# Optimization experiments

Measured on AMD Instinct MI355X. Metric: run time of the kernel, lower is better.

The kernel has to match this reference:

```python
import jax, jax.numpy as jnp
from jax import lax
import numpy as np

B, L, D = 16, 512, 256
F, K = 256, 3
M = 2048
EPS = 1e-5


def setup_inputs() -> dict:
    key = jax.random.key(0)
    ks = jax.random.split(key, 12)
    x = jax.random.normal(ks[0], (B, L, D), jnp.float32)
    # integer durations >= 1, sum over L <= 3*512 = 1536 < M, as in training targets
    target = jax.random.randint(ks[1], (B, L), 1, 4)
    s = 0.02
    conv1_w = jax.random.normal(ks[2], (F, D, K), jnp.float32) * s
    conv1_b = jnp.zeros((F,), jnp.float32)
    ln1_g = jnp.ones((F,), jnp.float32)
    ln1_b = jnp.zeros((F,), jnp.float32)
    conv2_w = jax.random.normal(ks[3], (F, F, K), jnp.float32) * s
    conv2_b = jnp.zeros((F,), jnp.float32)
    ln2_g = jnp.ones((F,), jnp.float32)
    ln2_b = jnp.zeros((F,), jnp.float32)
    lin_w = jax.random.normal(ks[4], (F, 1), jnp.float32) * s
    lin_b = jnp.zeros((1,), jnp.float32)
    return dict(x=x, target=target, mel_max_length=M,
                conv1_w=conv1_w, conv1_b=conv1_b, ln1_g=ln1_g, ln1_b=ln1_b,
                conv2_w=conv2_w, conv2_b=conv2_b, ln2_g=ln2_g, ln2_b=ln2_b,
                lin_w=lin_w, lin_b=lin_b)


def _layer_norm(h, g, b):
    mu = jnp.mean(h, axis=-1, keepdims=True)
    var = jnp.mean(jnp.square(h - mu), axis=-1, keepdims=True)
    return (h - mu) * lax.rsqrt(var + EPS) * g + b


def _conv1d(h_bld, w, b):
    # h: (B, L, C_in), w: (C_out, C_in, K) -> (B, L, C_out), SAME padding
    pad = (w.shape[-1] - 1) // 2
    h = jnp.transpose(h_bld, (0, 2, 1))  # (B, C, L)
    h = lax.conv_general_dilated(h, w, (1,), [(pad, pad)],
                                 dimension_numbers=('NCH', 'OIH', 'NCH'))
    return jnp.transpose(h + b[None, :, None], (0, 2, 1))


def _duration_predictor(x, conv1_w, conv1_b, ln1_g, ln1_b,
                        conv2_w, conv2_b, ln2_g, ln2_b, lin_w, lin_b):
    # FastSpeech duration predictor (eval mode: dropout = identity)
    h = jax.nn.relu(_layer_norm(_conv1d(x, conv1_w, conv1_b), ln1_g, ln1_b))
    h = jax.nn.relu(_layer_norm(_conv1d(h, conv2_w, conv2_b), ln2_g, ln2_b))
    return jax.nn.relu(h @ lin_w + lin_b)[..., 0]  # (B, L)


def _length_regulate(x, dur, mel_max_length):
    # alignment[b,m,l] = 1 iff cs[l-1] <= m < cs[l]  (exactly the scatter+diff trick
    # of create_alignment, padded to mel_max_length as in the original F.pad)
    cs = jnp.cumsum(dur, axis=1)              # (B, L) inclusive cumsum
    prev = cs - dur                           # exclusive cumsum
    m = jnp.arange(mel_max_length)[None, :, None]  # (1, M, 1)
    align = ((m >= prev[:, None, :]) & (m < cs[:, None, :])).astype(x.dtype)  # (B,M,L)
    return jnp.einsum('bml,bld->bmd', align, x)


def reference(x, target, mel_max_length, conv1_w, conv1_b, ln1_g, ln1_b,
              conv2_w, conv2_b, ln2_g, ln2_b, lin_w, lin_b):
    dup = _duration_predictor(x, conv1_w, conv1_b, ln1_g, ln1_b,
                              conv2_w, conv2_b, ln2_g, ln2_b, lin_w, lin_b)
    output = _length_regulate(x, target, mel_max_length)
    return (output, dup)
```

## Files before the change

kernel.cpp:

```cpp
#include <hip/hip_runtime.h>
#include <hip/hip_bf16.h>

#define Bn 16
#define Ln 512
#define Cn 256
#define Fn 256
#define Kn 3
#define Mn 2048

#define NKSTEP 24
#define MT 32
#define XS_PS 264
#define XROWS 50
#define HROWS 48
#define HOFF  8
#define NCONVBLK 256

typedef __attribute__((ext_vector_type(8))) short short8;
typedef __attribute__((ext_vector_type(4))) float f32x4;

static __device__ __forceinline__ unsigned short f2bf(float f) {
    unsigned int u = __float_as_uint(f);
    return (unsigned short)((u + 0x7fff + ((u >> 16) & 1)) >> 16);
}

__global__ __launch_bounds__(256) void pack_scan(
    const float* __restrict__ w1, const float* __restrict__ w2,
    unsigned short* __restrict__ bp1, unsigned short* __restrict__ bp2,
    const int* __restrict__ target, int* __restrict__ map)
{
    __shared__ int ss[256];
    const int blk = blockIdx.x;
    const int t = threadIdx.x;
    if (blk < 16) {
        const int bb = blk;
        int v0 = target[bb * Ln + 2 * t];
        int v1 = target[bb * Ln + 2 * t + 1];
        ss[t] = v0 + v1;
        __syncthreads();
        for (int off = 1; off < 256; off <<= 1) {
            int add = (t >= off) ? ss[t - off] : 0;
            __syncthreads();
            ss[t] += add;
            __syncthreads();
        }
        int S     = ss[t];
        int total = ss[255];
        int cs1   = S;
        int cs0   = S - v1;
        int prev0 = cs0 - v0;
        for (int m = prev0; m < cs0; ++m) map[bb * Mn + m] = 2 * t;
        for (int m = cs0;   m < cs1; ++m) map[bb * Mn + m] = 2 * t + 1;
        for (int m = total + t; m < Mn; m += 256) map[bb * Mn + m] = -1;
    } else {
        int v = (blk - 16) * 256 + t;
        const float* w = w1;
        unsigned short* bp = bp1;
        if (v >= 24576) { v -= 24576; w = w2; bp = bp2; }
        int lane = v & 63, nt = (v >> 6) & 15, s = v >> 10;
        int f    = nt * 16 + (lane & 15);
        int kap0 = s * 32 + (lane >> 4) * 8;
        const float* p = w + ((size_t)f * Cn + (kap0 & 255)) * Kn + (kap0 >> 8);
        short8 o;
        #pragma unroll
        for (int j = 0; j < 8; ++j) o[j] = (short)f2bf(p[3 * j]);
        *(short8*)(bp + (size_t)v * 8) = o;
    }
}

__global__ __launch_bounds__(256, 4) void conv12_gather(
    const float* __restrict__ x,
    const unsigned short* __restrict__ bp1,
    const unsigned short* __restrict__ bp2,
    const float* __restrict__ c1b, const float* __restrict__ g1, const float* __restrict__ be1,
    const float* __restrict__ c2b, const float* __restrict__ g2, const float* __restrict__ be2,
    const float* __restrict__ lw,  const float* __restrict__ lb,
    const int* __restrict__ gmap,
    float* __restrict__ out,
    float* __restrict__ dup)
{
    __shared__ __align__(16) unsigned short xs[XROWS * XS_PS];
    __shared__ float2 red[HROWS][4];
    __shared__ float  red2[MT][4];

    const int t = threadIdx.x;

    if (blockIdx.x >= NCONVBLK) {
        int e4 = (blockIdx.x - NCONVBLK) * 256 + t;
        int d4 = e4 & 63;
        int bm = e4 >> 6;
        int b  = bm >> 11;
        int l  = gmap[bm];
        float4 val = make_float4(0.f, 0.f, 0.f, 0.f);
        if (l >= 0) val = *((const float4*)(x + (size_t)(b * Ln + l) * Cn) + d4);
        ((float4*)out)[e4] = val;
        return;
    }

    const int b  = blockIdx.x >> 4;
    const int l0 = (blockIdx.x & 15) * MT;

    for (int idx = t; idx < XROWS * 64; idx += 256) {
        int row = idx >> 6;
        int c4  = (idx & 63) * 4;
        int l = l0 - 9 + row;
        float4 v = make_float4(0.f, 0.f, 0.f, 0.f);
        if (l >= 0 && l < Ln) v = *(const float4*)&x[((size_t)b * Ln + l) * Cn + c4];
        unsigned int lo = (unsigned int)f2bf(v.x) | ((unsigned int)f2bf(v.y) << 16);
        unsigned int hi = (unsigned int)f2bf(v.z) | ((unsigned int)f2bf(v.w) << 16);
        *(uint2*)&xs[row * XS_PS + c4] = make_uint2(lo, hi);
    }
    __syncthreads();

    const int lane = t & 63;
    const int wv   = t >> 6;
    const int mrow = lane & 15;
    const int q    = lane >> 4;

    f32x4  acc1[3][4] = {};
    short8 bfr[2][4];
    short8 afr[2][3];

    auto loadB1 = [&](int s, int slot) {
        const unsigned short* p = bp1 + (size_t)((s * 16 + wv * 4) * 64 + lane) * 8;
        #pragma unroll
        for (int i = 0; i < 4; ++i)
            bfr[slot][i] = *(const short8*)(p + (size_t)i * 64 * 8);
    };
    auto loadA1 = [&](int s, int slot) {
        const int k    = s >> 3;
        const int dcol = (s & 7) * 32 + q * 8;
        #pragma unroll
        for (int mt = 0; mt < 3; ++mt)
            afr[slot][mt] = *(const short8*)&xs[(mt * 16 + mrow + k) * XS_PS + dcol];
    };

    loadB1(0, 0); loadA1(0, 0);
    loadB1(1, 1); loadA1(1, 1);

    #pragma unroll 2
    for (int s = 0; s < NKSTEP; ++s) {
        const int slot = s & 1;
        #pragma unroll
        for (int mt = 0; mt < 3; ++mt)
            #pragma unroll
            for (int i = 0; i < 4; ++i)
                acc1[mt][i] = __builtin_amdgcn_mfma_f32_16x16x32_bf16(
                    afr[slot][mt], bfr[slot][i], acc1[mt][i], 0, 0, 0);
        const int sn = (s + 2 < NKSTEP) ? (s + 2) : s;
        loadB1(sn, slot);
        loadA1(sn, slot);
    }

    {
        float gv[4], bv[4], biasv[4];
        #pragma unroll
        for (int i = 0; i < 4; ++i) {
            int col = wv * 64 + i * 16 + mrow;
            biasv[i] = c1b[col];
            gv[i]    = g1[col];
            bv[i]    = be1[col];
        }
        #pragma unroll
        for (int mt = 0; mt < 3; ++mt)
            #pragma unroll
            for (int i = 0; i < 4; ++i)
                #pragma unroll
                for (int r = 0; r < 4; ++r)
                    acc1[mt][i][r] += biasv[i];

        #pragma unroll
        for (int mt = 0; mt < 3; ++mt)
            #pragma unroll
            for (int r = 0; r < 4; ++r) {
                float s  = acc1[mt][0][r] + acc1[mt][1][r] + acc1[mt][2][r] + acc1[mt][3][r];
                float sq = acc1[mt][0][r] * acc1[mt][0][r] + acc1[mt][1][r] * acc1[mt][1][r]
                         + acc1[mt][2][r] * acc1[mt][2][r] + acc1[mt][3][r] * acc1[mt][3][r];
                #pragma unroll
                for (int off = 1; off <= 8; off <<= 1) {
                    s  += __shfl_xor(s,  off, 64);
                    sq += __shfl_xor(sq, off, 64);
                }
                if (mrow == 0) red[mt * 16 + q * 4 + r][wv] = make_float2(s, sq);
            }
        __syncthreads();

        float muv[3][4], rsv[3][4];
        #pragma unroll
        for (int mt = 0; mt < 3; ++mt)
            #pragma unroll
            for (int r = 0; r < 4; ++r) {
                int row = mt * 16 + q * 4 + r;
                float2 p0 = red[row][0], p1 = red[row][1], p2 = red[row][2], p3 = red[row][3];
                float s  = p0.x + p1.x + p2.x + p3.x;
                float sq = p0.y + p1.y + p2.y + p3.y;
                float mu  = s * (1.f / 256.f);
                float var = sq * (1.f / 256.f) - mu * mu;
                muv[mt][r] = mu;
                rsv[mt][r] = rsqrtf(var + 1e-5f);
            }

        #pragma unroll
        for (int mt = 0; mt < 3; ++mt)
            #pragma unroll
            for (int r = 0; r < 4; ++r) {
                int jr = mt * 16 + q * 4 + r;
                int l  = l0 - HOFF + jr;
                bool ok = (l >= 0 && l < Ln);
                #pragma unroll
                for (int i = 0; i < 4; ++i) {
                    float o = ok ? fmaxf((acc1[mt][i][r] - muv[mt][r]) * rsv[mt][r] * gv[i] + bv[i], 0.f)
                                 : 0.f;
                    xs[jr * XS_PS + (wv * 64 + i * 16 + mrow)] = f2bf(o);
                }
            }
    }
    __syncthreads();

    f32x4  acc2[2][4] = {};
    short8 afr2[2][2];

    auto loadB2 = [&](int s, int slot) {
        const unsigned short* p = bp2 + (size_t)((s * 16 + wv * 4) * 64 + lane) * 8;
        #pragma unroll
        for (int i = 0; i < 4; ++i)
            bfr[slot][i] = *(const short8*)(p + (size_t)i * 64 * 8);
    };
    auto loadA2 = [&](int s, int slot) {
        const int k    = s >> 3;
        const int dcol = (s & 7) * 32 + q * 8;
        #pragma unroll
        for (int mt = 0; mt < 2; ++mt)
            afr2[slot][mt] = *(const short8*)&xs[(mt * 16 + mrow + k + 7) * XS_PS + dcol];
    };

    loadB2(0, 0); loadA2(0, 0);
    loadB2(1, 1); loadA2(1, 1);

    #pragma unroll 2
    for (int s = 0; s < NKSTEP; ++s) {
        const int slot = s & 1;
        #pragma unroll
        for (int mt = 0; mt < 2; ++mt)
            #pragma unroll
            for (int i = 0; i < 4; ++i)
                acc2[mt][i] = __builtin_amdgcn_mfma_f32_16x16x32_bf16(
                    afr2[slot][mt], bfr[slot][i], acc2[mt][i], 0, 0, 0);
        const int sn = (s + 2 < NKSTEP) ? (s + 2) : s;
        loadB2(sn, slot);
        loadA2(sn, slot);
    }

    {
        float gv[4], bv[4], biasv[4], lwv[4];
        #pragma unroll
        for (int i = 0; i < 4; ++i) {
            int col = wv * 64 + i * 16 + mrow;
            biasv[i] = c2b[col];
            gv[i]    = g2[col];
            bv[i]    = be2[col];
            lwv[i]   = lw[col];
        }
        #pragma unroll
        for (int mt = 0; mt < 2; ++mt)
            #pragma unroll
            for (int i = 0; i < 4; ++i)
                #pragma unroll
                for (int r = 0; r < 4; ++r)
                    acc2[mt][i][r] += biasv[i];

        #pragma unroll
        for (int mt = 0; mt < 2; ++mt)
            #pragma unroll
            for (int r = 0; r < 4; ++r) {
                float s  = acc2[mt][0][r] + acc2[mt][1][r] + acc2[mt][2][r] + acc2[mt][3][r];
                float sq = acc2[mt][0][r] * acc2[mt][0][r] + acc2[mt][1][r] * acc2[mt][1][r]
                         + acc2[mt][2][r] * acc2[mt][2][r] + acc2[mt][3][r] * acc2[mt][3][r];
                #pragma unroll
                for (int off = 1; off <= 8; off <<= 1) {
                    s  += __shfl_xor(s,  off, 64);
                    sq += __shfl_xor(sq, off, 64);
                }
                if (mrow == 0) red[mt * 16 + q * 4 + r][wv] = make_float2(s, sq);
            }
        __syncthreads();

        float muv[2][4], rsv[2][4];
        #pragma unroll
        for (int mt = 0; mt < 2; ++mt)
            #pragma unroll
            for (int r = 0; r < 4; ++r) {
                int row = mt * 16 + q * 4 + r;
                float2 p0 = red[row][0], p1 = red[row][1], p2 = red[row][2], p3 = red[row][3];
                float s  = p0.x + p1.x + p2.x + p3.x;
                float sq = p0.y + p1.y + p2.y + p3.y;
                float mu  = s * (1.f / 256.f);
                float var = sq * (1.f / 256.f) - mu * mu;
                muv[mt][r] = mu;
                rsv[mt][r] = rsqrtf(var + 1e-5f);
            }

        #pragma unroll
        for (int mt = 0; mt < 2; ++mt)
            #pragma unroll
            for (int r = 0; r < 4; ++r) {
                float dot = 0.f;
                #pragma unroll
                for (int i = 0; i < 4; ++i) {
                    float o = fmaxf((acc2[mt][i][r] - muv[mt][r]) * rsv[mt][r] * gv[i] + bv[i], 0.f);
                    dot += o * lwv[i];
                }
                #pragma unroll
                for (int off = 1; off <= 8; off <<= 1)
                    dot += __shfl_xor(dot, off, 64);
                if (mrow == 0) red2[mt * 16 + q * 4 + r][wv] = dot;
            }
        __syncthreads();
        if (t < MT) {
            float d = red2[t][0] + red2[t][1] + red2[t][2] + red2[t][3];
            dup[b * Ln + l0 + t] = fmaxf(d + lb[0], 0.f);
        }
    }
}

extern "C" void kernel_launch(void* const* d_in, const int* in_sizes, int n_in,
                              void* d_out, int out_size, void* d_ws, size_t ws_size,
                              hipStream_t stream) {
    const float* x    = (const float*)d_in[0];
    const int*   targ = (const int*)d_in[1];
    const float* c1w = (const float*)d_in[3];
    const float* c1b = (const float*)d_in[4];
    const float* g1  = (const float*)d_in[5];
    const float* be1 = (const float*)d_in[6];
    const float* c2w = (const float*)d_in[7];
    const float* c2b = (const float*)d_in[8];
    const float* g2  = (const float*)d_in[9];
    const float* be2 = (const float*)d_in[10];
    const float* lw  = (const float*)d_in[11];
    const float* lb  = (const float*)d_in[12];

    float* out     = (float*)d_out;
    float* out_dup = out + (size_t)Bn * Mn * Cn;

    char* ws = (char*)d_ws;
    unsigned short* bp1 = (unsigned short*)ws;
    unsigned short* bp2 = (unsigned short*)(ws + 393216);
    int*            map = (int*)(ws + 2 * 393216);

    pack_scan<<<208, 256, 0, stream>>>(c1w, c2w, bp1, bp2, targ, map);

    conv12_gather<<<NCONVBLK + (Bn * Mn * Cn / 4) / 256, 256, 0, stream>>>(
        x, bp1, bp2, c1b, g1, be1, c2b, g2, be2, lw, lb,
        map, out, out_dup);
}
```

Baseline: 132.7 us.

## Use 512-thread blocks: 8 waves split conv N-dim, gather does 4 float4 per thread

Doubles the block size to 512 threads so each conv block uses eight waves, each covering 32 output channels instead of 64. This halves per-wave accumulator and B-fragment registers, and the LayerNorm reductions now combine eight partials. The gather part shrinks from 8192 blocks to 1024, with each thread issuing four independent float4 gathers strided across the output. The aims are more wave-level parallelism in the conv and less block-launch overhead in the gather, at the cost of more redundant A-fragment LDS reads and wider cross-wave reductions.

Result: faster. 121.4 us (-8.5%).

```diff
diff --git a/kernel.cpp b/kernel.cpp
--- a/kernel.cpp
+++ b/kernel.cpp
@@ -15,6 +15,7 @@
 #define HROWS 48
 #define HOFF  8
 #define NCONVBLK 256
+#define NGATHERBLK 1024
 
 typedef __attribute__((ext_vector_type(8))) short short8;
 typedef __attribute__((ext_vector_type(4))) float f32x4;
@@ -68,7 +69,7 @@
     }
 }
 
-__global__ __launch_bounds__(256, 4) void conv12_gather(
+__global__ __launch_bounds__(512) void conv12_gather(
     const float* __restrict__ x,
     const unsigned short* __restrict__ bp1,
     const unsigned short* __restrict__ bp2,
@@ -80,27 +81,37 @@
     float* __restrict__ dup)
 {
     __shared__ __align__(16) unsigned short xs[XROWS * XS_PS];
-    __shared__ float2 red[HROWS][4];
-    __shared__ float  red2[MT][4];
+    __shared__ float2 red[HROWS][8];
+    __shared__ float  red2[MT][8];
 
     const int t = threadIdx.x;
 
     if (blockIdx.x >= NCONVBLK) {
-        int e4 = (blockIdx.x - NCONVBLK) * 256 + t;
-        int d4 = e4 & 63;
-        int bm = e4 >> 6;
-        int b  = bm >> 11;
-        int l  = gmap[bm];
-        float4 val = make_float4(0.f, 0.f, 0.f, 0.f);
-        if (l >= 0) val = *((const float4*)(x + (size_t)(b * Ln + l) * Cn) + d4);
-        ((float4*)out)[e4] = val;
+        const int base = (blockIdx.x - NCONVBLK) * 512 + t;
+        int lv[4];
+        #pragma unroll
+        for (int i = 0; i < 4; ++i)
+            lv[i] = gmap[(base + i * 524288) >> 6];
+        float4 val[4];
+        #pragma unroll
+        for (int i = 0; i < 4; ++i) {
+            int e4 = base + i * 524288;
+            int d4 = e4 & 63;
+            int b  = e4 >> 17;
+            val[i] = make_float4(0.f, 0.f, 0.f, 0.f);
+            if (lv[i] >= 0)
+                val[i] = *((const float4*)(x + (size_t)(b * Ln + lv[i]) * Cn) + d4);
+        }
+        #pragma unroll
+        for (int i = 0; i < 4; ++i)
+            ((float4*)out)[base + i * 524288] = val[i];
         return;
     }
 
     const int b  = blockIdx.x >> 4;
     const int l0 = (blockIdx.x & 15) * MT;
 
-    for (int idx = t; idx < XROWS * 64; idx += 256) {
+    for (int idx = t; idx < XROWS * 64; idx += 512) {
         int row = idx >> 6;
         int c4  = (idx & 63) * 4;
         int l = l0 - 9 + row;
@@ -117,46 +128,47 @@
     const int mrow = lane & 15;
     const int q    = lane >> 4;
 
-    f32x4  acc1[3][4] = {};
-    short8 bfr[2][4];
-    short8 afr[2][3];
-
-    auto loadB1 = [&](int s, int slot) {
-        const unsigned short* p = bp1 + (size_t)((s * 16 + wv * 4) * 64 + lane) * 8;
-        #pragma unroll
-        for (int i = 0; i < 4; ++i)
-            bfr[slot][i] = *(const short8*)(p + (size_t)i * 64 * 8);
-    };
-    auto loadA1 = [&](int s, int slot) {
-        const int k    = s >> 3;
-        const int dcol = (s & 7) * 32 + q * 8;
-        #pragma unroll
-        for (int mt = 0; mt < 3; ++mt)
-            afr[slot][mt] = *(const short8*)&xs[(mt * 16 + mrow + k) * XS_PS + dcol];
-    };
-
-    loadB1(0, 0); loadA1(0, 0);
-    loadB1(1, 1); loadA1(1, 1);
-
-    #pragma unroll 2
-    for (int s = 0; s < NKSTEP; ++s) {
-        const int slot = s & 1;
-        #pragma unroll
-        for (int mt = 0; mt < 3; ++mt)
-            #pragma unroll
-            for (int i = 0; i < 4; ++i)
-                acc1[mt][i] = __builtin_amdgcn_mfma_f32_16x16x32_bf16(
-                    afr[slot][mt], bfr[slot][i], acc1[mt][i], 0, 0, 0);
-        const int sn = (s + 2 < NKSTEP) ? (s + 2) : s;
-        loadB1(sn, slot);
-        loadA1(sn, slot);
-    }
-
+    f32x4  acc1[3][2] = {};
     {
-        float gv[4], bv[4], biasv[4];
-        #pragma unroll
-        for (int i = 0; i < 4; ++i) {
-            int col = wv * 64 + i * 16 + mrow;
+        short8 bfr[2][2];
+        short8 afr[2][3];
+
+        auto loadB1 = [&](int s, int slot) {
+            const unsigned short* p = bp1 + (size_t)((s * 16 + wv * 2) * 64 + lane) * 8;
+            bfr[slot][0] = *(const short8*)p;
+            bfr[slot][1] = *(const short8*)(p + 64 * 8);
+        };
+        auto loadA1 = [&](int s, int slot) {
+            const int k    = s >> 3;
+            const int dcol = (s & 7) * 32 + q * 8;
+            #pragma unroll
+            for (int mt = 0; mt < 3; ++mt)
+                afr[slot][mt] = *(const short8*)&xs[(mt * 16 + mrow + k) * XS_PS + dcol];
+        };
+
+        loadB1(0, 0); loadA1(0, 0);
+        loadB1(1, 1); loadA1(1, 1);
+
+        #pragma unroll 2
+        for (int s = 0; s < NKSTEP; ++s) {
+            const int slot = s & 1;
+            #pragma unroll
+            for (int mt = 0; mt < 3; ++mt)
+                #pragma unroll
+                for (int i = 0; i < 2; ++i)
+                    acc1[mt][i] = __builtin_amdgcn_mfma_f32_16x16x32_bf16(
+                        afr[slot][mt], bfr[slot][i], acc1[mt][i], 0, 0, 0);
+            const int sn = (s + 2 < NKSTEP) ? (s + 2) : s;
+            loadB1(sn, slot);
+            loadA1(sn, slot);
+        }
+    }
+
+    {
+        float gv[2], bv[2], biasv[2];
+        #pragma unroll
+        for (int i = 0; i < 2; ++i) {
+            int col = wv * 32 + i * 16 + mrow;
             biasv[i] = c1b[col];
             gv[i]    = g1[col];
             bv[i]    = be1[col];
@@ -164,7 +176,7 @@
         #pragma unroll
         for (int mt = 0; mt < 3; ++mt)
             #pragma unroll
-            for (int i = 0; i < 4; ++i)
+            for (int i = 0; i < 2; ++i)
                 #pragma unroll
                 for (int r = 0; r < 4; ++r)
                     acc1[mt][i][r] += biasv[i];
@@ -173,9 +185,8 @@
         for (int mt = 0; mt < 3; ++mt)
             #pragma unroll
             for (int r = 0; r < 4; ++r) {
-                float s  = acc1[mt][0][r] + acc1[mt][1][r] + acc1[mt][2][r] + acc1[mt][3][r];
-                float sq = acc1[mt][0][r] * acc1[mt][0][r] + acc1[mt][1][r] * acc1[mt][1][r]
-                         + acc1[mt][2][r] * acc1[mt][2][r] + acc1[mt][3][r] * acc1[mt][3][r];
+                float s  = acc1[mt][0][r] + acc1[mt][1][r];
+                float sq = acc1[mt][0][r] * acc1[mt][0][r] + acc1[mt][1][r] * acc1[mt][1][r];
                 #pragma unroll
                 for (int off = 1; off <= 8; off <<= 1) {
                     s  += __shfl_xor(s,  off, 64);
@@ -191,9 +202,12 @@
             #pragma unroll
             for (int r = 0; r < 4; ++r) {
                 int row = mt * 16 + q * 4 + r;
-                float2 p0 = red[row][0], p1 = red[row][1], p2 = red[row][2], p3 = red[row][3];
-                float s  = p0.x + p1.x + p2.x + p3.x;
-                float sq = p0.y + p1.y + p2.y + p3.y;
+                float s = 0.f, sq = 0.f;
+                #pragma unroll
+                for (int w = 0; w < 8; ++w) {
+                    float2 pp = red[row][w];
+                    s += pp.x; sq += pp.y;
+                }
                 float mu  = s * (1.f / 256.f);
                 float var = sq * (1.f / 256.f) - mu * mu;
                 muv[mt][r] = mu;
@@ -208,54 +222,56 @@
                 int l  = l0 - HOFF + jr;
                 bool ok = (l >= 0 && l < Ln);
                 #pragma unroll
-                for (int i = 0; i < 4; ++i) {
+                for (int i = 0; i < 2; ++i) {
                     float o = ok ? fmaxf((acc1[mt][i][r] - muv[mt][r]) * rsv[mt][r] * gv[i] + bv[i], 0.f)
                                  : 0.f;
-                    xs[jr * XS_PS + (wv * 64 + i * 16 + mrow)] = f2bf(o);
+                    xs[jr * XS_PS + (wv * 32 + i * 16 + mrow)] = f2bf(o);
                 }
             }
     }
     __syncthreads();
 
-    f32x4  acc2[2][4] = {};
-    short8 afr2[2][2];
-
-    auto loadB2 = [&](int s, int slot) {
-        const unsigned short* p = bp2 + (size_t)((s * 16 + wv * 4) * 64 + lane) * 8;
-        #pragma unroll
-        for (int i = 0; i < 4; ++i)
-            bfr[slot][i] = *(const short8*)(p + (size_t)i * 64 * 8);
-    };
-    auto loadA2 = [&](int s, int slot) {
-        const int k    = s >> 3;
-        const int dcol = (s & 7) * 32 + q * 8;
-        #pragma unroll
-        for (int mt = 0; mt < 2; ++mt)
-            afr2[slot][mt] = *(const short8*)&xs[(mt * 16 + mrow + k + 7) * XS_PS + dcol];
-    };
-
-    loadB2(0, 0); loadA2(0, 0);
-    loadB2(1, 1); loadA2(1, 1);
-
-    #pragma unroll 2
-    for (int s = 0; s < NKSTEP; ++s) {
-        const int slot = s & 1;
-        #pragma unroll
-        for (int mt = 0; mt < 2; ++mt)
-            #pragma unroll
-            for (int i = 0; i < 4; ++i)
-                acc2[mt][i] = __builtin_amdgcn_mfma_f32_16x16x32_bf16(
-                    afr2[slot][mt], bfr[slot][i], acc2[mt][i], 0, 0, 0);
-        const int sn = (s + 2 < NKSTEP) ? (s + 2) : s;
-        loadB2(sn, slot);
-        loadA2(sn, slot);
-    }
-
+    f32x4  acc2[2][2] = {};
     {
-        float gv[4], bv[4], biasv[4], lwv[4];
-        #pragma unroll
-        for (int i = 0; i < 4; ++i) {
-            int col = wv * 64 + i * 16 + mrow;
+        short8 bfr[2][2];
+        short8 afr[2][2];
+
+        auto loadB2 = [&](int s, int slot) {
+            const unsigned short* p = bp2 + (size_t)((s * 16 + wv * 2) * 64 + lane) * 8;
+            bfr[slot][0] = *(const short8*)p;
+            bfr[slot][1] = *(const short8*)(p + 64 * 8);
+        };
+        auto loadA2 = [&](int s, int slot) {
+            const int k    = s >> 3;
+            const int dcol = (s & 7) * 32 + q * 8;
+            #pragma unroll
+            for (int mt = 0; mt < 2; ++mt)
+                afr[slot][mt] = *(const short8*)&xs[(mt * 16 + mrow + k + 7) * XS_PS + dcol];
+        };
+
+        loadB2(0, 0); loadA2(0, 0);
+        loadB2(1, 1); loadA2(1, 1);
+
+        #pragma unroll 2
+        for (int s = 0; s < NKSTEP; ++s) {
+            const int slot = s & 1;
+            #pragma unroll
+            for (int mt = 0; mt < 2; ++mt)
+                #pragma unroll
+                for (int i = 0; i < 2; ++i)
+                    acc2[mt][i] = __builtin_amdgcn_mfma_f32_16x16x32_bf16(
+                        afr[slot][mt], bfr[slot][i], acc2[mt][i], 0, 0, 0);
+            const int sn = (s + 2 < NKSTEP) ? (s + 2) : s;
+            loadB2(sn, slot);
+            loadA2(sn, slot);
+        }
+    }
+
+    {
+        float gv[2], bv[2], biasv[2], lwv[2];
+        #pragma unroll
+        for (int i = 0; i < 2; ++i) {
+            int col = wv * 32 + i * 16 + mrow;
             biasv[i] = c2b[col];
             gv[i]    = g2[col];
             bv[i]    = be2[col];
@@ -264,7 +280,7 @@
         #pragma unroll
         for (int mt = 0; mt < 2; ++mt)
             #pragma unroll
-            for (int i = 0; i < 4; ++i)
+            for (int i = 0; i < 2; ++i)
                 #pragma unroll
                 for (int r = 0; r < 4; ++r)
                     acc2[mt][i][r] += biasv[i];
@@ -273,9 +289,8 @@
         for (int mt = 0; mt < 2; ++mt)
             #pragma unroll
             for (int r = 0; r < 4; ++r) {
-                float s  = acc2[mt][0][r] + acc2[mt][1][r] + acc2[mt][2][r] + acc2[mt][3][r];
-                float sq = acc2[mt][0][r] * acc2[mt][0][r] + acc2[mt][1][r] * acc2[mt][1][r]
-                         + acc2[mt][2][r] * acc2[mt][2][r] + acc2[mt][3][r] * acc2[mt][3][r];
+                float s  = acc2[mt][0][r] + acc2[mt][1][r];
+                float sq = acc2[mt][0][r] * acc2[mt][0][r] + acc2[mt][1][r] * acc2[mt][1][r];
                 #pragma unroll
                 for (int off = 1; off <= 8; off <<= 1) {
                     s  += __shfl_xor(s,  off, 64);
@@ -291,9 +306,12 @@
             #pragma unroll
             for (int r = 0; r < 4; ++r) {
                 int row = mt * 16 + q * 4 + r;
-                float2 p0 = red[row][0], p1 = red[row][1], p2 = red[row][2], p3 = red[row][3];
-                float s  = p0.x + p1.x + p2.x + p3.x;
-                float sq = p0.y + p1.y + p2.y + p3.y;
+                float s = 0.f, sq = 0.f;
+                #pragma unroll
+                for (int w = 0; w < 8; ++w) {
+                    float2 pp = red[row][w];
+                    s += pp.x; sq += pp.y;
+                }
                 float mu  = s * (1.f / 256.f);
                 float var = sq * (1.f / 256.f) - mu * mu;
                 muv[mt][r] = mu;
@@ -306,7 +324,7 @@
             for (int r = 0; r < 4; ++r) {
                 float dot = 0.f;
                 #pragma unroll
-                for (int i = 0; i < 4; ++i) {
+                for (int i = 0; i < 2; ++i) {
                     float o = fmaxf((acc2[mt][i][r] - muv[mt][r]) * rsv[mt][r] * gv[i] + bv[i], 0.f);
                     dot += o * lwv[i];
                 }
@@ -317,7 +335,8 @@
             }
         __syncthreads();
         if (t < MT) {
-            float d = red2[t][0] + red2[t][1] + red2[t][2] + red2[t][3];
+            float d = red2[t][0] + red2[t][1] + red2[t][2] + red2[t][3]
+                    + red2[t][4] + red2[t][5] + red2[t][6] + red2[t][7];
             dup[b * Ln + l0 + t] = fmaxf(d + lb[0], 0.f);
         }
     }
@@ -349,7 +368,7 @@
 
     pack_scan<<<208, 256, 0, stream>>>(c1w, c2w, bp1, bp2, targ, map);
 
-    conv12_gather<<<NCONVBLK + (Bn * Mn * Cn / 4) / 256, 256, 0, stream>>>(
+    conv12_gather<<<NCONVBLK + NGATHERBLK, 512, 0, stream>>>(
         x, bp1, bp2, c1b, g1, be1, c2b, g2, be2, lw, lb,
         map, out, out_dup);
 }
```
